# Kernel tuning notes

Measured on AMD Instinct MI355X. Metric: run time of the kernel, lower is better.

Reference implementation:

```python
import jax, jax.numpy as jnp
import numpy as np

B, H, W = 16, 512, 512


def _nmax(a, pad_val):
    """Max over 3x3 cross (4-neighborhood + center), constant-padded borders."""
    p = jnp.pad(a, ((0, 0), (1, 1), (1, 1)), constant_values=pad_val)
    return jnp.maximum(a, jnp.maximum(
        jnp.maximum(p[:, :-2, 1:-1], p[:, 2:, 1:-1]),
        jnp.maximum(p[:, 1:-1, :-2], p[:, 1:-1, 2:])))


def _dilate(b):
    # cv2 dilate with 3x3 MORPH_ELLIPSE (== cross), border treated as background
    return _nmax(b, 0.0)


def _erode(b):
    # cv2 erode default border value == foreground, so erode = 1 - dilate(1 - b)
    return 1.0 - _nmax(1.0 - b, 0.0)


def setup_inputs() -> dict:
    key = jax.random.key(0)
    x = jax.random.uniform(key, (B, 4, H, W), dtype=jnp.float32)
    return {"x": x}


def reference(x):
    # --- majority vote with disagreement fallback to pred1 ---
    p1 = (x[:, 1] > 0.5).astype(jnp.float32)
    p2 = (x[:, 2] > 0.5).astype(jnp.float32)
    p3 = (x[:, 3] > 0.5).astype(jnp.float32)
    vote = p1 + p2 + p3
    m = jnp.where(vote >= 2, 1.0, jnp.where(vote == 1, p1, 0.0))

    # --- morphology: MORPH_CLOSE then MORPH_OPEN with 3x3 ellipse (cross) ---
    m = _erode(_dilate(m))   # close
    m = _dilate(_erode(m))   # open

    # --- 4-connected CCL (scipy ndimage.label default) via label propagation ---
    Bm, Hm, Wm = m.shape
    mask_i = m > 0
    init = jnp.where(mask_i,
                     jnp.arange(1, Hm * Wm + 1, dtype=jnp.int32).reshape(1, Hm, Wm),
                     jnp.int32(0))

    def cond(s):
        return s[1]

    def body(s):
        lbl, _ = s
        new = jnp.where(mask_i, _nmax(lbl, 0), 0)
        return (new, jnp.any(new != lbl))

    lbl, _ = jax.lax.while_loop(cond, body, (init, jnp.array(True)))

    # --- component sizes and small-component removal ---
    sizes = jax.vmap(lambda mm, ll: jax.ops.segment_sum(
        mm.ravel(), ll.ravel(), num_segments=Hm * Wm + 1))(m, lbl)
    min_size = max(50, int(0.001 * Hm * Wm))  # = 262 for 512x512
    keep = jnp.take_along_axis(sizes, lbl.reshape(Bm, -1), axis=1)
    keep = (keep.reshape(Bm, Hm, Wm) > min_size).astype(jnp.float32)
    m = m * keep
    return m[:, None, :, :]  # [B, 1, H, W]
```

## Files before the change

kernel.cpp:

```cpp
#include <hip/hip_runtime.h>

typedef unsigned long long u64;
typedef unsigned u32;
typedef unsigned char u8;

#define BATCH 16
#define Hh 512
#define Ww 512
#define IMG (Hh * Ww)
#define TOT (BATCH * IMG)
#define WPI 4096
#define WROW 8
#define NWORDS (TOT / 64)
#define MIN_SIZE 262
#define MAXRUNS (NWORDS * 32)

#define BAND 8
#define HALO 4
#define BROWS (BAND + 2 * HALO)
#define BWORDS (BROWS * WROW)
#define MAXBRUNS (64 * 32)

__device__ __forceinline__ u32 runstart(u64 bits, int s) {
    u64 ms = (s >= 63) ? ~0ULL : ((1ULL << (s + 1)) - 1);
    u64 nz = ~bits & ms;
    return nz ? (u32)(64 - __clzll(nz)) : 0u;
}
__device__ __forceinline__ u32 runlen(u64 bits, int s) {
    u64 v = ~(bits >> s);
    return v ? (u32)(__ffsll(v) - 1) : (u32)(64 - s);
}
__device__ __forceinline__ u32 runrank(u64 bits, u64 st, int s) {
    u32 rs = runstart(bits, s);
    return (u32)__popcll(st & (((u64)1 << rs) - 1));
}

__device__ __forceinline__ u64 morph_word(const u64* M, int w, int rr, bool er) {
    const u64 B = er ? ~0ULL : 0ULL;
    int wx = w & 7;
    u64 cc = M[w];
    u64 lf = (cc << 1) | (wx > 0 ? (M[w - 1] >> 63) : (er ? 1ULL : 0ULL));
    u64 rt = (cc >> 1) | (wx < 7 ? (M[w + 1] << 63) : (er ? (1ULL << 63) : 0ULL));
    u64 up = (rr <= 0)      ? B : (w >= WROW          ? M[w - WROW] : B);
    u64 dn = (rr >= Hh - 1) ? B : (w < BWORDS - WROW  ? M[w + WROW] : B);
    return er ? (cc & lf & rt & up & dn) : (cc | lf | rt | up | dn);
}

template <typename P>
__device__ __forceinline__ u32 uf_find_halve(P L, u32 x) {
    while (true) {
        u32 p = L[x];
        if (p == x) return x;
        u32 gp = L[p];
        if (gp == p) return p;
        atomicMin(&L[x], gp);
        x = gp;
    }
}
template <typename P>
__device__ __forceinline__ void uf_merge(P L, u32 a, u32 b) {
    while (true) {
        a = uf_find_halve(L, a);
        b = uf_find_halve(L, b);
        if (a == b) return;
        if (a > b) { u32 t = a; a = b; b = t; }
        u32 old = atomicMin(&L[b], a);
        if (old == b) return;
        b = old;
    }
}

__global__ __launch_bounds__(256) void vote_pack_kernel(const float4* __restrict__ x4,
                                                        u64* __restrict__ mp0,
                                                        u32* __restrict__ runCtr) {
    int t = threadIdx.x, blk = blockIdx.x;
    if (blk == 0 && t == 0) *runCtr = 0u;
    int img = blk >> 6;
    size_t p4 = (size_t)((blk & 63) * 4096 + t * 16) >> 2;
    const float4* c1 = x4 + ((size_t)img * 4 + 1) * (IMG / 4);
    const float4* c2 = x4 + ((size_t)img * 4 + 2) * (IMG / 4);
    const float4* c3 = x4 + ((size_t)img * 4 + 3) * (IMG / 4);
    u32 m = 0;
    #pragma unroll
    for (int q = 0; q < 4; ++q) {
        float4 a1 = c1[p4 + q], a2 = c2[p4 + q], a3 = c3[p4 + q];
        u32 b0 = (a1.x > 0.5f) | ((a2.x > 0.5f) & (a3.x > 0.5f));
        u32 b1 = (a1.y > 0.5f) | ((a2.y > 0.5f) & (a3.y > 0.5f));
        u32 b2 = (a1.z > 0.5f) | ((a2.z > 0.5f) & (a3.z > 0.5f));
        u32 b3 = (a1.w > 0.5f) | ((a2.w > 0.5f) & (a3.w > 0.5f));
        m |= (b0 | (b1 << 1) | (b2 << 2) | (b3 << 3)) << (q * 4);
    }
    u32 w32 = m | (__shfl_xor(m, 1) << 16);
    u64 w = (u64)w32 | ((u64)__shfl_xor(w32, 2) << 32);
    if ((t & 3) == 0) mp0[(size_t)blk * 64 + (t >> 2)] = w;
}

__global__ __launch_bounds__(256) void morph_ccl_kernel(const u64* __restrict__ mp0,
                                                        u64* __restrict__ mp,
                                                        u32* __restrict__ L,
                                                        u32* __restrict__ wordbase,
                                                        u32* __restrict__ counts,
                                                        u8*  __restrict__ len8,
                                                        u32* __restrict__ runCtr) {
    __shared__ u64 Ma[BWORDS], Mb[BWORDS];
    __shared__ u32 Ll[MAXBRUNS];
    __shared__ u32 wb_l[64];
    __shared__ u32 baseSh, totSh;
    int blk = blockIdx.x;
    int img = blk >> 6;
    int r0  = (blk & 63) * BAND;
    int t = threadIdx.x;
    int rr = r0 - HALO + (t >> 3);

    if (t < BWORDS)
        Ma[t] = (rr >= 0 && rr < Hh) ? mp0[(size_t)img * WPI + (size_t)rr * WROW + (t & 7)] : 0;
    __syncthreads();

    if (t < BWORDS) Mb[t] = morph_word(Ma, t, rr, false);
    __syncthreads();
    if (t < BWORDS) Ma[t] = morph_word(Mb, t, rr, true);
    __syncthreads();
    if (t < BWORDS) Mb[t] = morph_word(Ma, t, rr, true);
    __syncthreads();
    if (t < BWORDS) Ma[t] = morph_word(Mb, t, rr, false);
    __syncthreads();

    if (t < 64)
        mp[(size_t)img * WPI + (size_t)r0 * WROW + t] = Ma[32 + t];

    u32 myexcl = 0;
    if (t < 64) {
        u64 bits = Ma[32 + t];
        u64 st = bits & ~(bits << 1);
        u32 cnt = __popcll(st);
        u32 inc = cnt;
        #pragma unroll
        for (int d = 1; d < 64; d <<= 1) {
            u32 v = __shfl_up(inc, d);
            if (t >= d) inc += v;
        }
        myexcl = inc - cnt;
        if (t == 63) { baseSh = atomicAdd(runCtr, inc); totSh = inc; }
    }
    __syncthreads();
    u32 base = baseSh, tot = totSh;
    if (t < 64) {
        wb_l[t] = myexcl;
        wordbase[(size_t)img * WPI + (size_t)r0 * WROW + t] = base + myexcl;
    }
    for (u32 i = t; i < tot; i += 256) { Ll[i] = i; counts[base + i] = 0u; }
    __syncthreads();

    if (t < 56) {
        int rp = t >> 3, w = t & 7;
        u64 a = Ma[32 + rp * 8 + w], b = Ma[32 + (rp + 1) * 8 + w];
        u64 ov = a & b, seg = ov & ~(ov << 1);
        if (seg) {
            u64 sta = a & ~(a << 1), stb = b & ~(b << 1);
            u32 ba = wb_l[rp * 8 + w], bb = wb_l[(rp + 1) * 8 + w];
            while (seg) {
                int s = __ffsll(seg) - 1; seg &= seg - 1;
                uf_merge((u32*)Ll, ba + runrank(a, sta, s), bb + runrank(b, stb, s));
            }
        }
    } else if (t >= 64 && t < 120) {
        int ht = t - 64;
        int r = ht / 7, w = 1 + ht % 7;
        u64 a = Ma[32 + r * 8 + w - 1], b = Ma[32 + r * 8 + w];
        if ((a >> 63) & b & 1ULL) {
            u64 sta = a & ~(a << 1);
            uf_merge((u32*)Ll, wb_l[r * 8 + w - 1] + (u32)__popcll(sta & ~(1ULL << 63)) - 1u
                                 + (u32)((sta >> 63) & 1ULL),
                               wb_l[r * 8 + w]);
        }
    }
    __syncthreads();

    if (t < 64) {
        u64 bits = Ma[32 + t];
        u64 st = bits & ~(bits << 1);
        u32 local = wb_l[t];
        while (st) {
            int s = __ffsll(st) - 1; st &= st - 1;
            u32 r = local, p = Ll[r];
            while (p != r) { r = p; p = Ll[r]; }
            L[base + local] = base + r;
            len8[base + local] = (u8)runlen(bits, s);
            local++;
        }
    }
}

#define BITEMS (BATCH * 63 * WROW)
__global__ void border_merge_kernel(const u64* __restrict__ mp,
                                    const u32* __restrict__ wordbase, u32* L) {
    int e = blockIdx.x * blockDim.x + threadIdx.x;
    if (e >= BITEMS) return;
    int w = e & 7, k = (e >> 3) % 63 + 1, img = e / (63 * 8);
    int R = k * BAND;
    size_t wa_i = (size_t)img * WPI + (size_t)(R - 1) * WROW + w;
    size_t wb_i = (size_t)img * WPI + (size_t)R * WROW + w;
    u64 a = mp[wa_i], b = mp[wb_i];
    u64 ov = a & b, seg = ov & ~(ov << 1);
    if (!seg) return;
    u64 sta = a & ~(a << 1), stb = b & ~(b << 1);
    u32 wba = wordbase[wa_i], wbb = wordbase[wb_i];
    while (seg) {
        int s = __ffsll(seg) - 1; seg &= seg - 1;
        uf_merge(L, wba + runrank(a, sta, s), wbb + runrank(b, stb, s));
    }
}

#define ACCUM_STRIDE (1024 * 256)
__global__ __launch_bounds__(256) void accum_kernel(u32* __restrict__ L,
                                                    const u8* __restrict__ len8,
                                                    u32* __restrict__ counts,
                                                    const u32* __restrict__ runCtr) {
    u32 n = *runCtr;
    u32 gid = blockIdx.x * 256 + threadIdx.x;
    int tid = threadIdx.x;
    u32 trips = (n + ACCUM_STRIDE - 1) / ACCUM_STRIDE;
    for (u32 k = 0; k < trips; ++k) {
        u32 id = gid + k * ACCUM_STRIDE;
        bool valid = id < n;
        u32 r = 0xFFFFFFFFu, len = 0;
        if (valid) {
            r = id; u32 p = L[r];
            while (p != r) { r = p; p = L[r]; }
            L[id] = r;
            len = len8[id];
        }
        bool pending = true;
        while (true) {
            u64 act = __ballot(pending);
            if (!act) break;
            int leader = __ffsll(act) - 1;
            u32 lr = __shfl(r, leader);
            bool mine = pending && (r == lr);
            u32 c = mine ? len : 0u;
            c += __shfl_xor(c, 32); c += __shfl_xor(c, 16); c += __shfl_xor(c, 8);
            c += __shfl_xor(c, 4);  c += __shfl_xor(c, 2);  c += __shfl_xor(c, 1);
            if ((tid & 63) == leader && lr != 0xFFFFFFFFu) atomicAdd(&counts[lr], c);
            if (mine) pending = false;
        }
    }
}

__global__ __launch_bounds__(256) void final_kernel(const u64* __restrict__ mp,
                                                    const u32* __restrict__ wordbase,
                                                    const u32* __restrict__ L,
                                                    const u32* __restrict__ counts,
                                                    float* __restrict__ out) {
    __shared__ u64 km[256];
    int tid = threadIdx.x;
    int widx = blockIdx.x * 256 + tid;
    u64 bits = mp[widx];
    u64 st = bits & ~(bits << 1);
    u32 id = wordbase[widx];
    u64 keep = 0;
    while (st) {
        int s = __ffsll(st) - 1; st &= st - 1;
        u32 r = L[id++];
        if (counts[r] > MIN_SIZE) {
            u32 len = runlen(bits, s);
            keep |= (len == 64 ? ~0ULL : ((1ULL << len) - 1ULL)) << s;
        }
    }
    km[tid] = keep;
    __syncthreads();
    float4* o4 = (float4*)out + (size_t)blockIdx.x * 4096;
    for (int i = tid; i < 4096; i += 256) {
        u32 nib = (u32)(km[i >> 4] >> ((i & 15) * 4)) & 0xFu;
        o4[i] = make_float4(nib & 1u ? 1.f : 0.f, nib & 2u ? 1.f : 0.f,
                            nib & 4u ? 1.f : 0.f, nib & 8u ? 1.f : 0.f);
    }
}

extern "C" void kernel_launch(void* const* d_in, const int* in_sizes, int n_in,
                              void* d_out, int out_size, void* d_ws, size_t ws_size,
                              hipStream_t stream) {
    const float* x = (const float*)d_in[0];
    float* out = (float*)d_out;

    u64* mp0 = (u64*)d_ws;
    u64* mp  = mp0 + NWORDS;
    u32* wordbase = (u32*)(mp + NWORDS);
    u32* L      = wordbase + NWORDS;
    u32* counts = L + MAXRUNS;
    u8*  len8   = (u8*)(counts + MAXRUNS);
    u32* runCtr = (u32*)(len8 + MAXRUNS);

    const int block = 256;

    vote_pack_kernel<<<1024, block, 0, stream>>>((const float4*)x, mp0, runCtr);
    morph_ccl_kernel<<<BATCH * 64, block, 0, stream>>>(mp0, mp, L, wordbase, counts, len8, runCtr);
    border_merge_kernel<<<(BITEMS + block - 1) / block, block, 0, stream>>>(mp, wordbase, L);
    accum_kernel<<<1024, block, 0, stream>>>(L, len8, counts, runCtr);
    final_kernel<<<NWORDS / block, block, 0, stream>>>(mp, wordbase, L, counts, out);
}
```

Measured before the change: 78.07 us.

## Fuse vote/pack into morphology band kernel and use fixed per-band run slots

```diff
diff --git a/kernel.cpp b/kernel.cpp
--- a/kernel.cpp
+++ b/kernel.cpp
@@ -13,13 +13,14 @@
 #define WROW 8
 #define NWORDS (TOT / 64)
 #define MIN_SIZE 262
-#define MAXRUNS (NWORDS * 32)
 
 #define BAND 8
 #define HALO 4
 #define BROWS (BAND + 2 * HALO)
 #define BWORDS (BROWS * WROW)
-#define MAXBRUNS (64 * 32)
+#define MAXBRUNS 2048
+#define NBANDS (BATCH * 64)
+#define TOTSLOTS (NBANDS * MAXBRUNS)
 
 __device__ __forceinline__ u32 runstart(u64 bits, int s) {
     u64 ms = (s >= 63) ? ~0ULL : ((1ULL << (s + 1)) - 1);
@@ -70,52 +71,51 @@
     }
 }
 
-__global__ __launch_bounds__(256) void vote_pack_kernel(const float4* __restrict__ x4,
-                                                        u64* __restrict__ mp0,
-                                                        u32* __restrict__ runCtr) {
-    int t = threadIdx.x, blk = blockIdx.x;
-    if (blk == 0 && t == 0) *runCtr = 0u;
-    int img = blk >> 6;
-    size_t p4 = (size_t)((blk & 63) * 4096 + t * 16) >> 2;
-    const float4* c1 = x4 + ((size_t)img * 4 + 1) * (IMG / 4);
-    const float4* c2 = x4 + ((size_t)img * 4 + 2) * (IMG / 4);
-    const float4* c3 = x4 + ((size_t)img * 4 + 3) * (IMG / 4);
-    u32 m = 0;
-    #pragma unroll
-    for (int q = 0; q < 4; ++q) {
-        float4 a1 = c1[p4 + q], a2 = c2[p4 + q], a3 = c3[p4 + q];
-        u32 b0 = (a1.x > 0.5f) | ((a2.x > 0.5f) & (a3.x > 0.5f));
-        u32 b1 = (a1.y > 0.5f) | ((a2.y > 0.5f) & (a3.y > 0.5f));
-        u32 b2 = (a1.z > 0.5f) | ((a2.z > 0.5f) & (a3.z > 0.5f));
-        u32 b3 = (a1.w > 0.5f) | ((a2.w > 0.5f) & (a3.w > 0.5f));
-        m |= (b0 | (b1 << 1) | (b2 << 2) | (b3 << 3)) << (q * 4);
-    }
-    u32 w32 = m | (__shfl_xor(m, 1) << 16);
-    u64 w = (u64)w32 | ((u64)__shfl_xor(w32, 2) << 32);
-    if ((t & 3) == 0) mp0[(size_t)blk * 64 + (t >> 2)] = w;
-}
-
-__global__ __launch_bounds__(256) void morph_ccl_kernel(const u64* __restrict__ mp0,
+__global__ __launch_bounds__(256) void morph_ccl_kernel(const float4* __restrict__ x4,
                                                         u64* __restrict__ mp,
                                                         u32* __restrict__ L,
                                                         u32* __restrict__ wordbase,
                                                         u32* __restrict__ counts,
                                                         u8*  __restrict__ len8,
-                                                        u32* __restrict__ runCtr) {
+                                                        u32* __restrict__ bandTot) {
     __shared__ u64 Ma[BWORDS], Mb[BWORDS];
     __shared__ u32 Ll[MAXBRUNS];
     __shared__ u32 wb_l[64];
-    __shared__ u32 baseSh, totSh;
+    __shared__ u32 totSh;
     int blk = blockIdx.x;
     int img = blk >> 6;
     int r0  = (blk & 63) * BAND;
     int t = threadIdx.x;
+
+    {
+        const float4* c1 = x4 + ((size_t)img * 4 + 1) * (IMG / 4);
+        const float4* c2 = x4 + ((size_t)img * 4 + 2) * (IMG / 4);
+        const float4* c3 = x4 + ((size_t)img * 4 + 3) * (IMG / 4);
+        #pragma unroll
+        for (int pass = 0; pass < 2; ++pass) {
+            int wpx = pass * 4096 + t * 16;
+            int rr  = r0 - HALO + (wpx >> 9);
+            u32 m = 0;
+            if (rr >= 0 && rr < Hh) {
+                size_t p4 = ((size_t)rr * Ww + (wpx & 511)) >> 2;
+                #pragma unroll
+                for (int q = 0; q < 4; ++q) {
+                    float4 a1 = c1[p4 + q], a2 = c2[p4 + q], a3 = c3[p4 + q];
+                    u32 b0 = (a1.x > 0.5f) | ((a2.x > 0.5f) & (a3.x > 0.5f));
+                    u32 b1 = (a1.y > 0.5f) | ((a2.y > 0.5f) & (a3.y > 0.5f));
+                    u32 b2 = (a1.z > 0.5f) | ((a2.z > 0.5f) & (a3.z > 0.5f));
+                    u32 b3 = (a1.w > 0.5f) | ((a2.w > 0.5f) & (a3.w > 0.5f));
+                    m |= (b0 | (b1 << 1) | (b2 << 2) | (b3 << 3)) << (q * 4);
+                }
+            }
+            u32 w32 = m | (__shfl_xor(m, 1) << 16);
+            u64 w = (u64)w32 | ((u64)__shfl_xor(w32, 2) << 32);
+            if ((t & 3) == 0) Ma[pass * 64 + (t >> 2)] = w;
+        }
+    }
+    __syncthreads();
+
     int rr = r0 - HALO + (t >> 3);
-
-    if (t < BWORDS)
-        Ma[t] = (rr >= 0 && rr < Hh) ? mp0[(size_t)img * WPI + (size_t)rr * WROW + (t & 7)] : 0;
-    __syncthreads();
-
     if (t < BWORDS) Mb[t] = morph_word(Ma, t, rr, false);
     __syncthreads();
     if (t < BWORDS) Ma[t] = morph_word(Mb, t, rr, true);
@@ -128,6 +128,7 @@
     if (t < 64)
         mp[(size_t)img * WPI + (size_t)r0 * WROW + t] = Ma[32 + t];
 
+    u32 base = (u32)blk * MAXBRUNS;
     u32 myexcl = 0;
     if (t < 64) {
         u64 bits = Ma[32 + t];
@@ -140,14 +141,15 @@
             if (t >= d) inc += v;
         }
         myexcl = inc - cnt;
-        if (t == 63) { baseSh = atomicAdd(runCtr, inc); totSh = inc; }
-    }
-    __syncthreads();
-    u32 base = baseSh, tot = totSh;
+        if (t == 63) totSh = inc;
+    }
+    __syncthreads();
+    u32 tot = totSh;
     if (t < 64) {
         wb_l[t] = myexcl;
         wordbase[(size_t)img * WPI + (size_t)r0 * WROW + t] = base + myexcl;
     }
+    if (t == 0) bandTot[blk] = tot;
     for (u32 i = t; i < tot; i += 256) { Ll[i] = i; counts[base + i] = 0u; }
     __syncthreads();
 
@@ -211,18 +213,16 @@
     }
 }
 
-#define ACCUM_STRIDE (1024 * 256)
 __global__ __launch_bounds__(256) void accum_kernel(u32* __restrict__ L,
                                                     const u8* __restrict__ len8,
                                                     u32* __restrict__ counts,
-                                                    const u32* __restrict__ runCtr) {
-    u32 n = *runCtr;
+                                                    const u32* __restrict__ bandTot) {
     u32 gid = blockIdx.x * 256 + threadIdx.x;
     int tid = threadIdx.x;
-    u32 trips = (n + ACCUM_STRIDE - 1) / ACCUM_STRIDE;
-    for (u32 k = 0; k < trips; ++k) {
-        u32 id = gid + k * ACCUM_STRIDE;
-        bool valid = id < n;
+    #pragma unroll
+    for (int k = 0; k < TOTSLOTS / (1024 * 256); ++k) {
+        u32 id = gid + (u32)k * (1024 * 256);
+        bool valid = (id & (MAXBRUNS - 1)) < bandTot[id >> 11];
         u32 r = 0xFFFFFFFFu, len = 0;
         if (valid) {
             r = id; u32 p = L[r];
@@ -282,19 +282,18 @@
     const float* x = (const float*)d_in[0];
     float* out = (float*)d_out;
 
-    u64* mp0 = (u64*)d_ws;
-    u64* mp  = mp0 + NWORDS;
+    u64* mp = (u64*)d_ws;
     u32* wordbase = (u32*)(mp + NWORDS);
-    u32* L      = wordbase + NWORDS;
-    u32* counts = L + MAXRUNS;
-    u8*  len8   = (u8*)(counts + MAXRUNS);
-    u32* runCtr = (u32*)(len8 + MAXRUNS);
+    u32* L       = wordbase + NWORDS;
+    u32* counts  = L + TOTSLOTS;
+    u8*  len8    = (u8*)(counts + TOTSLOTS);
+    u32* bandTot = (u32*)(len8 + TOTSLOTS);
 
     const int block = 256;
 
-    vote_pack_kernel<<<1024, block, 0, stream>>>((const float4*)x, mp0, runCtr);
-    morph_ccl_kernel<<<BATCH * 64, block, 0, stream>>>(mp0, mp, L, wordbase, counts, len8, runCtr);
+    morph_ccl_kernel<<<NBANDS, block, 0, stream>>>((const float4*)x, mp, L,
+                                                   wordbase, counts, len8, bandTot);
     border_merge_kernel<<<(BITEMS + block - 1) / block, block, 0, stream>>>(mp, wordbase, L);
-    accum_kernel<<<1024, block, 0, stream>>>(L, len8, counts, runCtr);
+    accum_kernel<<<1024, block, 0, stream>>>(L, len8, counts, bandTot);
     final_kernel<<<NWORDS / block, block, 0, stream>>>(mp, wordbase, L, counts, out);
 }
```

New measurement: 86.35 us. 1.11x slower.

## Fuse border merge into morph_ccl via last-arriver flags per band boundary

Applied to the files above, without the earlier changes.

```diff
diff --git a/kernel.cpp b/kernel.cpp
--- a/kernel.cpp
+++ b/kernel.cpp
@@ -20,6 +20,7 @@
 #define BROWS (BAND + 2 * HALO)
 #define BWORDS (BROWS * WROW)
 #define MAXBRUNS (64 * 32)
+#define NBANDS (BATCH * 64)
 
 __device__ __forceinline__ u32 runstart(u64 bits, int s) {
     u64 ms = (s >= 63) ? ~0ULL : ((1ULL << (s + 1)) - 1);
@@ -72,9 +73,11 @@
 
 __global__ __launch_bounds__(256) void vote_pack_kernel(const float4* __restrict__ x4,
                                                         u64* __restrict__ mp0,
-                                                        u32* __restrict__ runCtr) {
+                                                        u32* __restrict__ runCtr,
+                                                        u32* __restrict__ bflag) {
     int t = threadIdx.x, blk = blockIdx.x;
     if (blk == 0 && t == 0) *runCtr = 0u;
+    if (t == 0) bflag[blk] = 0u;
     int img = blk >> 6;
     size_t p4 = (size_t)((blk & 63) * 4096 + t * 16) >> 2;
     const float4* c1 = x4 + ((size_t)img * 4 + 1) * (IMG / 4);
@@ -101,11 +104,12 @@
                                                         u32* __restrict__ wordbase,
                                                         u32* __restrict__ counts,
                                                         u8*  __restrict__ len8,
-                                                        u32* __restrict__ runCtr) {
+                                                        u32* __restrict__ runCtr,
+                                                        u32* __restrict__ bflag) {
     __shared__ u64 Ma[BWORDS], Mb[BWORDS];
     __shared__ u32 Ll[MAXBRUNS];
     __shared__ u32 wb_l[64];
-    __shared__ u32 baseSh, totSh;
+    __shared__ u32 baseSh, totSh, doTopSh, doBotSh;
     int blk = blockIdx.x;
     int img = blk >> 6;
     int r0  = (blk & 63) * BAND;
@@ -189,25 +193,37 @@
             local++;
         }
     }
-}
-
-#define BITEMS (BATCH * 63 * WROW)
-__global__ void border_merge_kernel(const u64* __restrict__ mp,
-                                    const u32* __restrict__ wordbase, u32* L) {
-    int e = blockIdx.x * blockDim.x + threadIdx.x;
-    if (e >= BITEMS) return;
-    int w = e & 7, k = (e >> 3) % 63 + 1, img = e / (63 * 8);
-    int R = k * BAND;
-    size_t wa_i = (size_t)img * WPI + (size_t)(R - 1) * WROW + w;
-    size_t wb_i = (size_t)img * WPI + (size_t)R * WROW + w;
-    u64 a = mp[wa_i], b = mp[wb_i];
-    u64 ov = a & b, seg = ov & ~(ov << 1);
-    if (!seg) return;
-    u64 sta = a & ~(a << 1), stb = b & ~(b << 1);
-    u32 wba = wordbase[wa_i], wbb = wordbase[wb_i];
-    while (seg) {
-        int s = __ffsll(seg) - 1; seg &= seg - 1;
-        uf_merge(L, wba + runrank(a, sta, s), wbb + runrank(b, stb, s));
+
+    __threadfence();
+    __syncthreads();
+    if (t == 0) {
+        doTopSh = 0u; doBotSh = 0u;
+        if ((blk & 63) != 0)  doTopSh = (atomicAdd(&bflag[blk], 1u) == 1u);
+        if ((blk & 63) != 63) doBotSh = (atomicAdd(&bflag[blk + 1], 1u) == 1u);
+    }
+    __syncthreads();
+    u32 doTop = doTopSh, doBot = doBotSh;
+    if ((doTop || doBot)) {
+        __threadfence();
+        if (t < 16) {
+            int which = t >> 3;
+            if ((which == 0 && doTop) || (which == 1 && doBot)) {
+                int R = which == 0 ? r0 : r0 + BAND;
+                int w = t & 7;
+                size_t wa_i = (size_t)img * WPI + (size_t)(R - 1) * WROW + w;
+                size_t wb_i = wa_i + WROW;
+                u64 a = mp[wa_i], b = mp[wb_i];
+                u64 ov = a & b, seg = ov & ~(ov << 1);
+                if (seg) {
+                    u64 sta = a & ~(a << 1), stb = b & ~(b << 1);
+                    u32 wba = wordbase[wa_i], wbb = wordbase[wb_i];
+                    while (seg) {
+                        int s = __ffsll(seg) - 1; seg &= seg - 1;
+                        uf_merge(L, wba + runrank(a, sta, s), wbb + runrank(b, stb, s));
+                    }
+                }
+            }
+        }
     }
 }
 
@@ -289,12 +305,13 @@
     u32* counts = L + MAXRUNS;
     u8*  len8   = (u8*)(counts + MAXRUNS);
     u32* runCtr = (u32*)(len8 + MAXRUNS);
+    u32* bflag  = runCtr + 1;
 
     const int block = 256;
 
-    vote_pack_kernel<<<1024, block, 0, stream>>>((const float4*)x, mp0, runCtr);
-    morph_ccl_kernel<<<BATCH * 64, block, 0, stream>>>(mp0, mp, L, wordbase, counts, len8, runCtr);
-    border_merge_kernel<<<(BITEMS + block - 1) / block, block, 0, stream>>>(mp, wordbase, L);
+    vote_pack_kernel<<<1024, block, 0, stream>>>((const float4*)x, mp0, runCtr, bflag);
+    morph_ccl_kernel<<<NBANDS, block, 0, stream>>>(mp0, mp, L, wordbase, counts,
+                                                   len8, runCtr, bflag);
     accum_kernel<<<1024, block, 0, stream>>>(L, len8, counts, runCtr);
     final_kernel<<<NWORDS / block, block, 0, stream>>>(mp, wordbase, L, counts, out);
 }
```

Measured after the change: 201.4 us. +158.0%, slower.

## Pre-aggregate component sizes per band and accumulate only over band-local roots

Applied to the files above, without the earlier changes.

```diff
diff --git a/kernel.cpp b/kernel.cpp
--- a/kernel.cpp
+++ b/kernel.cpp
@@ -2,7 +2,6 @@
 
 typedef unsigned long long u64;
 typedef unsigned u32;
-typedef unsigned char u8;
 
 #define BATCH 16
 #define Hh 512
@@ -14,12 +13,14 @@
 #define NWORDS (TOT / 64)
 #define MIN_SIZE 262
 #define MAXRUNS (NWORDS * 32)
+#define RCAP (1u << 20)
 
 #define BAND 8
 #define HALO 4
 #define BROWS (BAND + 2 * HALO)
 #define BWORDS (BROWS * WROW)
 #define MAXBRUNS (64 * 32)
+#define NBANDS (BATCH * 64)
 
 __device__ __forceinline__ u32 runstart(u64 bits, int s) {
     u64 ms = (s >= 63) ? ~0ULL : ((1ULL << (s + 1)) - 1);
@@ -72,9 +73,9 @@
 
 __global__ __launch_bounds__(256) void vote_pack_kernel(const float4* __restrict__ x4,
                                                         u64* __restrict__ mp0,
-                                                        u32* __restrict__ runCtr) {
+                                                        u32* __restrict__ ctrs) {
     int t = threadIdx.x, blk = blockIdx.x;
-    if (blk == 0 && t == 0) *runCtr = 0u;
+    if (blk == 0 && t == 0) { ctrs[0] = 0u; ctrs[1] = 0u; }
     int img = blk >> 6;
     size_t p4 = (size_t)((blk & 63) * 4096 + t * 16) >> 2;
     const float4* c1 = x4 + ((size_t)img * 4 + 1) * (IMG / 4);
@@ -100,12 +101,13 @@
                                                         u32* __restrict__ L,
                                                         u32* __restrict__ wordbase,
                                                         u32* __restrict__ counts,
-                                                        u8*  __restrict__ len8,
-                                                        u32* __restrict__ runCtr) {
+                                                        u32* __restrict__ rootIds,
+                                                        u32* __restrict__ ctrs) {
     __shared__ u64 Ma[BWORDS], Mb[BWORDS];
     __shared__ u32 Ll[MAXBRUNS];
+    __shared__ u32 szl[MAXBRUNS];
     __shared__ u32 wb_l[64];
-    __shared__ u32 baseSh, totSh;
+    __shared__ u32 baseSh, totSh, baseRSh;
     int blk = blockIdx.x;
     int img = blk >> 6;
     int r0  = (blk & 63) * BAND;
@@ -140,7 +142,7 @@
             if (t >= d) inc += v;
         }
         myexcl = inc - cnt;
-        if (t == 63) { baseSh = atomicAdd(runCtr, inc); totSh = inc; }
+        if (t == 63) { baseSh = atomicAdd(&ctrs[0], inc); totSh = inc; }
     }
     __syncthreads();
     u32 base = baseSh, tot = totSh;
@@ -148,7 +150,7 @@
         wb_l[t] = myexcl;
         wordbase[(size_t)img * WPI + (size_t)r0 * WROW + t] = base + myexcl;
     }
-    for (u32 i = t; i < tot; i += 256) { Ll[i] = i; counts[base + i] = 0u; }
+    for (u32 i = t; i < tot; i += 256) { Ll[i] = i; szl[i] = 0u; }
     __syncthreads();
 
     if (t < 56) {
@@ -185,7 +187,43 @@
             u32 r = local, p = Ll[r];
             while (p != r) { r = p; p = Ll[r]; }
             L[base + local] = base + r;
-            len8[base + local] = (u8)runlen(bits, s);
+            atomicAdd(&szl[r], runlen(bits, s));
+            local++;
+        }
+    }
+    __syncthreads();
+
+    u32 cntR = 0;
+    if (t < 64) {
+        u64 bits = Ma[32 + t];
+        u64 st = bits & ~(bits << 1);
+        u32 local = wb_l[t];
+        while (st) { st &= st - 1; if (Ll[local] == local) cntR++; local++; }
+    }
+    u32 myexclR = 0;
+    if (t < 64) {
+        u32 incR = cntR;
+        #pragma unroll
+        for (int d = 1; d < 64; d <<= 1) {
+            u32 v = __shfl_up(incR, d);
+            if (t >= d) incR += v;
+        }
+        myexclR = incR - cntR;
+        if (t == 63) baseRSh = incR ? atomicAdd(&ctrs[1], incR) : 0u;
+    }
+    __syncthreads();
+    if (t < 64 && cntR) {
+        u64 bits = Ma[32 + t];
+        u64 st = bits & ~(bits << 1);
+        u32 local = wb_l[t];
+        u32 j = baseRSh + myexclR;
+        while (st) {
+            st &= st - 1;
+            if (Ll[local] == local) {
+                if (j < RCAP) rootIds[j] = base + local;
+                counts[base + local] = szl[local];
+                j++;
+            }
             local++;
         }
     }
@@ -211,38 +249,18 @@
     }
 }
 
-#define ACCUM_STRIDE (1024 * 256)
 __global__ __launch_bounds__(256) void accum_kernel(u32* __restrict__ L,
-                                                    const u8* __restrict__ len8,
                                                     u32* __restrict__ counts,
-                                                    const u32* __restrict__ runCtr) {
-    u32 n = *runCtr;
-    u32 gid = blockIdx.x * 256 + threadIdx.x;
-    int tid = threadIdx.x;
-    u32 trips = (n + ACCUM_STRIDE - 1) / ACCUM_STRIDE;
-    for (u32 k = 0; k < trips; ++k) {
-        u32 id = gid + k * ACCUM_STRIDE;
-        bool valid = id < n;
-        u32 r = 0xFFFFFFFFu, len = 0;
-        if (valid) {
-            r = id; u32 p = L[r];
-            while (p != r) { r = p; p = L[r]; }
-            L[id] = r;
-            len = len8[id];
-        }
-        bool pending = true;
-        while (true) {
-            u64 act = __ballot(pending);
-            if (!act) break;
-            int leader = __ffsll(act) - 1;
-            u32 lr = __shfl(r, leader);
-            bool mine = pending && (r == lr);
-            u32 c = mine ? len : 0u;
-            c += __shfl_xor(c, 32); c += __shfl_xor(c, 16); c += __shfl_xor(c, 8);
-            c += __shfl_xor(c, 4);  c += __shfl_xor(c, 2);  c += __shfl_xor(c, 1);
-            if ((tid & 63) == leader && lr != 0xFFFFFFFFu) atomicAdd(&counts[lr], c);
-            if (mine) pending = false;
-        }
+                                                    const u32* __restrict__ rootIds,
+                                                    const u32* __restrict__ ctrs) {
+    u32 n = ctrs[1]; if (n > RCAP) n = RCAP;
+    u32 stride = 1024 * 256;
+    for (u32 idx = blockIdx.x * 256 + threadIdx.x; idx < n; idx += stride) {
+        u32 id = rootIds[idx];
+        u32 r = id, p = L[r];
+        while (p != r) { r = p; p = L[r]; }
+        L[id] = r;
+        if (r != id) atomicAdd(&counts[r], counts[id]);
     }
 }
 
@@ -260,7 +278,8 @@
     u64 keep = 0;
     while (st) {
         int s = __ffsll(st) - 1; st &= st - 1;
-        u32 r = L[id++];
+        u32 rb = L[id++];
+        u32 r  = L[rb];
         if (counts[r] > MIN_SIZE) {
             u32 len = runlen(bits, s);
             keep |= (len == 64 ? ~0ULL : ((1ULL << len) - 1ULL)) << s;
@@ -285,16 +304,17 @@
     u64* mp0 = (u64*)d_ws;
     u64* mp  = mp0 + NWORDS;
     u32* wordbase = (u32*)(mp + NWORDS);
-    u32* L      = wordbase + NWORDS;
-    u32* counts = L + MAXRUNS;
-    u8*  len8   = (u8*)(counts + MAXRUNS);
-    u32* runCtr = (u32*)(len8 + MAXRUNS);
+    u32* L       = wordbase + NWORDS;
+    u32* counts  = L + MAXRUNS;
+    u32* rootIds = counts + MAXRUNS;
+    u32* ctrs    = rootIds + RCAP;
 
     const int block = 256;
 
-    vote_pack_kernel<<<1024, block, 0, stream>>>((const float4*)x, mp0, runCtr);
-    morph_ccl_kernel<<<BATCH * 64, block, 0, stream>>>(mp0, mp, L, wordbase, counts, len8, runCtr);
+    vote_pack_kernel<<<1024, block, 0, stream>>>((const float4*)x, mp0, ctrs);
+    morph_ccl_kernel<<<NBANDS, block, 0, stream>>>(mp0, mp, L, wordbase, counts,
+                                                   rootIds, ctrs);
     border_merge_kernel<<<(BITEMS + block - 1) / block, block, 0, stream>>>(mp, wordbase, L);
-    accum_kernel<<<1024, block, 0, stream>>>(L, len8, counts, runCtr);
+    accum_kernel<<<1024, block, 0, stream>>>(L, counts, rootIds, ctrs);
     final_kernel<<<NWORDS / block, block, 0, stream>>>(mp, wordbase, L, counts, out);
 }
```

Measured after the change: 80.76 us. 1.03x slower.
